# Kernel optimization log

Measured on AMD Instinct MI355X. Metric: run time of the kernel, lower is better.

## Reference

```python
import jax, jax.numpy as jnp
import numpy as np

# Architecture constants (match init_kwargs)
J_OCT, Q, K = 4, 8, 7
DECIMATION, POOLING, INDEX = 2, 8, 0
NF = K * 2 ** J_OCT            # 112 taps per filter (kernel size / time grid length)
NSC = J_OCT * Q                # 32 wavelet scales (complex filters)
POOL_W = POOLING // DECIMATION ** (INDEX + 1)  # 4


def complex_hermite_interp(xi, xk, m, p):
    # xi: (NF,) time grid; xk: (NSC, K) knots; m, p: (2, K) values/derivatives
    h = jnp.array([[1., 0., -3., 2.], [0., 1., -2., 1.],
                   [0., 0., 3., -2.], [0., 0., -1., 1.]], dtype=xi.dtype)
    xx = jnp.stack([xk[:, :-1], xk[:, 1:]], axis=2)            # (NSC, K-1, 2)
    mm = jnp.stack([m[:, :-1], m[:, 1:]], axis=2)              # (2, K-1, 2)
    pp = jnp.stack([p[:, :-1], p[:, 1:]], axis=2)
    y = jnp.concatenate([mm, pp], axis=2)                      # (2, K-1, 4)
    yh = jnp.einsum('iab,bc->iac', y, h)                       # (2, K-1, 4)
    # normalized position in each knot interval: (NSC, K-1, NF)
    xn = (xi[None, None, :] - xx[:, :, 0:1]) / (xx[:, :, 1:2] - xx[:, :, 0:1])
    mask = ((xn >= 0.) & (xn < 1.)).astype(xi.dtype)
    xp = xn[..., None] ** jnp.arange(4, dtype=xi.dtype)        # (NSC, K-1, NF, 4)
    return jnp.einsum('irf,srtf->ist', yh, xp * mask[..., None])  # (2, NSC, NF)


def get_filters(m, p, scales_delta, knots_base):
    scales = 2. ** (jnp.arange(NSC, dtype=jnp.float32) / np.float32(Q)) + scales_delta
    clipped = jnp.clip(knots_base[None, :] * scales[:, None], 1., float(NF - K))
    knots_sum = jnp.cumsum(clipped, axis=1) - clipped          # exclusive cumsum
    knots = knots_sum - (K // 2) * scales[:, None]             # (NSC, K)
    time_max = np.float32(K * 2 ** (J_OCT - 1))
    time_grid = jnp.linspace(-time_max, time_max, NF)
    mask = jnp.ones((1, K), dtype=jnp.float32).at[0, 0].set(0.).at[0, -1].set(0.)
    m_null = m - jnp.mean(m[:, 1:-1], axis=1, keepdims=True)
    f = complex_hermite_interp(time_grid, knots, m_null * mask, p * mask)  # (2, NSC, NF)
    f = f / jnp.max(f, axis=2, keepdims=True)
    filt_concat = f.reshape(2 * NSC, NF)  # [real; imag] rows, same as tf.concat axis=0
    return jnp.transpose(filt_concat)[:, None, :]              # (NF, 1, 2*NSC) = WIO


def scatter_conv(x, kernel):
    B, C, T = x.shape
    xr = x.reshape(B * C, T, 1)
    xp = jnp.pad(xr, ((0, 0), (NF // 2 - 1, NF // 2 + 1), (0, 0)), mode='symmetric')
    return jax.lax.conv_general_dilated(
        xp, kernel, window_strides=(DECIMATION,), padding='VALID',
        dimension_numbers=('NWC', 'WIO', 'NWC'))                # (B*C, To, 2*NSC)


def reference(x, m, p, scales_delta, knots_base):
    B, C, T = x.shape
    kernel = get_filters(m, p, scales_delta, knots_base)
    x_conv, vjp = jax.vjp(lambda xx: scatter_conv(xx, kernel), x)
    u = jnp.sqrt(jnp.square(x_conv[..., :NSC]) + jnp.square(x_conv[..., NSC:]))  # (B*C, To, NSC)
    out_u = jnp.swapaxes(u.reshape(B, C, NSC, -1), 1, 2)       # (B, NSC, C, To)
    pooled = jax.lax.reduce_window(u, 0., jax.lax.add,
                                   (1, POOL_W, 1), (1, POOL_W, 1), 'VALID') / POOL_W
    pooled = jnp.swapaxes(pooled, 1, 2)                        # (B*C, NSC, Tp)
    out_s = pooled.reshape(B, C, NSC, -1)                      # (B, C, NSC, Tp)
    # embedded tf.gradients auxiliary reconstruction loss
    inverse = vjp(x_conv)[0]
    loss = jnp.mean(jnp.square(inverse - jax.lax.stop_gradient(x)))
    return out_u, out_s, loss


def setup_inputs() -> dict:
    key = jax.random.key(0)
    B, C, T = 16, 3, 65536
    x = jax.random.normal(key, (B, C, T), dtype=jnp.float32)
    n = jnp.arange(K, dtype=jnp.float32)
    ham = 0.54 - 0.46 * jnp.cos(2. * jnp.pi * n / K)           # periodic hamming (tf default)
    alt = jnp.cos(n * jnp.pi) * ham
    m = jnp.stack([alt, jnp.zeros(K, jnp.float32)])
    p = jnp.stack([jnp.zeros(K, jnp.float32), alt])
    scales_delta = jnp.zeros(NSC, dtype=jnp.float32)
    knots_base = jnp.ones(K, dtype=jnp.float32)
    return {'x': x, 'm': m, 'p': p, 'scales_delta': scales_delta, 'knots_base': knots_base}
```

## Files before the change

### kernel.cpp

```cpp
#include <hip/hip_runtime.h>

#define TLEN 65536
#define XPLEN 65648
#define TO 32769
#define OU_SIZE 50333184

typedef __attribute__((ext_vector_type(8))) short short8v;
typedef __attribute__((ext_vector_type(4))) float float4v;

__device__ __forceinline__ float fetch_xp(const float* __restrict__ xr, int idx) {
    int p = idx - 55;
    p = (p < 0) ? (-1 - p) : p;
    p = (p >= TLEN) ? (2 * TLEN - 1 - p) : p;
    return xr[p];
}

__device__ __forceinline__ ushort f2bf(float f) {
    unsigned u = __float_as_uint(f);
    unsigned r = (u + 0x7fffu + ((u >> 16) & 1u)) >> 16;
    return (ushort)r;
}

__device__ __forceinline__ void bar_lds() {
    __builtin_amdgcn_sched_barrier(0);
    asm volatile("s_waitcnt lgkmcnt(0)" ::: "memory");
    __builtin_amdgcn_s_barrier();
    __builtin_amdgcn_sched_barrier(0);
}

__global__ __launch_bounds__(256) void k1_filters(
    const float* __restrict__ m, const float* __restrict__ p,
    const float* __restrict__ sd, const float* __restrict__ kb,
    float* __restrict__ Wout, ushort* __restrict__ Wtb)
{
    __shared__ float knots[32][8];
    __shared__ float yh[2][6][4];
    __shared__ float fv[2][32][112];
    __shared__ float mx[64];
    __shared__ float mv[2][7], pv[2][7];
    int tid = threadIdx.x;
    if (tid < 32) {
        float s = exp2f((float)tid * 0.125f) + sd[tid];
        float cum = 0.f;
        for (int k = 0; k < 7; ++k) {
            float c = fminf(fmaxf(kb[k] * s, 1.f), 105.f);
            knots[tid][k] = cum - 3.f * s;
            cum += c;
        }
    }
    if (tid < 2) {
        float mean = 0.f;
        for (int k = 1; k <= 5; ++k) mean += m[tid * 7 + k];
        mean *= 0.2f;
        for (int k = 0; k < 7; ++k) {
            float msk = (k == 0 || k == 6) ? 0.f : 1.f;
            mv[tid][k] = (m[tid * 7 + k] - mean) * msk;
            pv[tid][k] = p[tid * 7 + k] * msk;
        }
    }
    __syncthreads();
    if (tid < 12) {
        int i = tid / 6, kk = tid % 6;
        float y0 = mv[i][kk], y1 = mv[i][kk + 1], y2 = pv[i][kk], y3 = pv[i][kk + 1];
        yh[i][kk][0] = y0;
        yh[i][kk][1] = y1;
        yh[i][kk][2] = -3.f * y0 - 2.f * y1 + 3.f * y2 - y3;
        yh[i][kk][3] = 2.f * y0 + y1 - 2.f * y2 + y3;
    }
    __syncthreads();
    for (int idx = tid; idx < 7168; idx += 256) {
        int i = idx / 3584, s = (idx / 112) % 32, fi = idx % 112;
        float xi = -56.f + (float)fi * (112.f / 111.f);
        float val = 0.f;
        for (int kk = 0; kk < 6; ++kk) {
            float x0 = knots[s][kk], x1 = knots[s][kk + 1];
            float xn = (xi - x0) / (x1 - x0);
            if (xn >= 0.f && xn < 1.f) {
                val += ((yh[i][kk][3] * xn + yh[i][kk][2]) * xn + yh[i][kk][1]) * xn + yh[i][kk][0];
            }
        }
        fv[i][s][fi] = val;
    }
    __syncthreads();
    if (tid < 64) {
        int i = tid >> 5, s = tid & 31;
        float mm_ = -1e30f;
        for (int fi = 0; fi < 112; ++fi) mm_ = fmaxf(mm_, fv[i][s][fi]);
        mx[tid] = mm_;
    }
    __syncthreads();
    for (int idx = tid; idx < 7168; idx += 256) {
        int i = idx / 3584, s = (idx / 112) % 32, fi = idx % 112;
        int o = i * 32 + s;
        Wout[fi * 64 + o] = fv[i][s][fi] / mx[o];
    }
    for (int idx = tid; idx < 8192; idx += 256) {
        int o = idx >> 7, k = idx & 127;
        float val = (k < 112) ? fv[o >> 5][o & 31][k] / mx[o] : 0.f;
        Wtb[idx] = f2bf(val);
    }
}

__global__ __launch_bounds__(256) void k1b_A(const float* __restrict__ W, float* __restrict__ A)
{
    int idx = blockIdx.x * 256 + threadIdx.x;
    if (idx >= 12544) return;
    int j = idx / 112, k = idx % 112;
    float s = 0.f;
    for (int o = 0; o < 64; ++o) s += W[j * 64 + o] * W[k * 64 + o];
    A[idx] = s;
}

__global__ __launch_bounds__(256) void k1c_C(const float* __restrict__ A, float* __restrict__ C)
{
    int idx = blockIdx.x * 256 + threadIdx.x;
    if (idx >= 448) return;
    int q = idx / 224, dd = idx % 224;
    int d = dd - 111;
    float s = 0.f;
    for (int k = q; k < 112; k += 2) {
        int jj = k + d;
        if (jj >= 0 && jj < 112) s += A[jj * 112 + k];
    }
    C[idx] = s;
}

__global__ __launch_bounds__(256) void k2k3_fused(
    const float* __restrict__ x, const ushort* __restrict__ Wtb,
    const float* __restrict__ Cg,
    float* __restrict__ out_u, float* __restrict__ out_s,
    double* __restrict__ part)
{
    __shared__ __align__(16) ushort xraw[2][384];
    __shared__ float ub[256][33];
    __shared__ float pb[32][65];
    __shared__ __align__(16) float sx[1248];
    __shared__ __align__(16) float Cl[448];
    __shared__ double wred[4];
    int row = blockIdx.y;
    int b = row / 3, c = row % 3;
    const float* xr = x + row * TLEN;
    int tid = threadIdx.x;
    int l = tid & 63, w = tid >> 6;
    int r16 = l & 15, kg = l >> 4;

    union U8 { short8v v; uint u[4]; uint4 q; };

    const ushort* WB = Wtb + r16 * 128 + 8 * kg;
    U8 wreg[4][4];
#pragma unroll
    for (int n = 0; n < 4; ++n)
#pragma unroll
        for (int ks = 0; ks < 4; ++ks)
            wreg[n][ks].q = *(const uint4*)(WB + n * 2048 + 32 * ks);

    int ebase = 2 * (32 * w + r16) + 8 * kg;

    int tstart = blockIdx.x * 8;
    int tend = (blockIdx.x == 31) ? 257 : (tstart + 8);
    int ntiles = tend - tstart;

    auto flush = [&](int f) {
        int slot = (f & 1) << 7;
        int pend_t0 = (tstart + f) * 128;
        const int NE = 128;
        for (int i = tid; i < (NE << 3); i += 256) {
            int r = i & 31;
            int g = i >> 5;
            size_t gb = ((size_t)((b * 32 + r) * 3 + c)) * TO + pend_t0;
            int pad = (int)((4 - (gb & 3)) & 3);
            int e = pad + (g << 2);
            if (e + 3 < NE) {
                int t = pend_t0 + e;
                float4 v = make_float4(ub[slot + e][r], ub[slot + e + 1][r],
                                       ub[slot + e + 2][r], ub[slot + e + 3][r]);
                if (t + 3 < TO) {
                    *(float4*)(out_u + gb + e) = v;
                } else {
                    if (t     < TO) out_u[gb + e]     = v.x;
                    if (t + 1 < TO) out_u[gb + e + 1] = v.y;
                    if (t + 2 < TO) out_u[gb + e + 2] = v.z;
                    if (t + 3 < TO) out_u[gb + e + 3] = v.w;
                }
            }
        }
        if (tid < 128) {
            int r = tid >> 2, j = tid & 3;
            size_t gb = ((size_t)((b * 32 + r) * 3 + c)) * TO + pend_t0;
            int pad = (int)((4 - (gb & 3)) & 3);
            if (pad > 0) {
                int G4 = ((NE - pad) >> 2) << 2;
                int e = (j < pad) ? j : (pad + G4 + (j - pad));
                if (e < NE) {
                    int t = pend_t0 + e;
                    if (t < TO) out_u[gb + e] = ub[slot + e][r];
                }
            }
        }
        int ps = (f & 1) << 5;
        int tp0 = pend_t0 >> 2;
        {
            int r = tid & 31;
            int g = tid >> 5;
            int tp = g << 2;
            size_t sb = ((size_t)(row * 32 + r)) * 8192 + tp0;
            if (tp0 + tp + 3 < 8192) {
                float4 v = make_float4(pb[r][ps + tp], pb[r][ps + tp + 1],
                                       pb[r][ps + tp + 2], pb[r][ps + tp + 3]);
                *(float4*)(out_s + sb + tp) = v;
            } else {
#pragma unroll
                for (int j = 0; j < 4; ++j)
                    if (tp0 + tp + j < 8192) out_s[sb + tp + j] = pb[r][ps + tp + j];
            }
        }
    };

    {
        int i0 = 2 * tstart * 128 + tid;
        float v0 = (i0 < XPLEN) ? fetch_xp(xr, i0) : 0.f;
        float v1 = 0.f;
        if (tid < 128) {
            int i1 = i0 + 256;
            v1 = (i1 < XPLEN) ? fetch_xp(xr, i1) : 0.f;
        }
        xraw[0][tid] = f2bf(v0);
        if (tid < 128) xraw[0][tid + 256] = f2bf(v1);
    }
    bar_lds();

    for (int it = 0; it < ntiles; ++it) {
        int half = it & 1;
        float n0 = 0.f, n1 = 0.f;
        bool hn = (it + 1 < ntiles);
        if (hn) {
            int i0 = 2 * (tstart + it + 1) * 128 + tid;
            n0 = (i0 < XPLEN) ? fetch_xp(xr, i0) : 0.f;
            if (tid < 128) {
                int i1 = i0 + 256;
                n1 = (i1 < XPLEN) ? fetch_xp(xr, i1) : 0.f;
            }
        }
        __builtin_amdgcn_sched_barrier(0);
        if (it >= 1) flush(it - 1);
        __builtin_amdgcn_sched_barrier(0);
        if (hn) {
            xraw[(it + 1) & 1][tid] = f2bf(n0);
            if (tid < 128) xraw[(it + 1) & 1][tid + 256] = f2bf(n1);
        }
        bar_lds();

        const ushort* xcur = xraw[half];
        float4v acc[2][4];
#pragma unroll
        for (int mt = 0; mt < 2; ++mt)
#pragma unroll
            for (int n = 0; n < 4; ++n)
                acc[mt][n] = (float4v){0.f, 0.f, 0.f, 0.f};

#pragma unroll
        for (int ks = 0; ks < 4; ++ks) {
            U8 a0, a1;
            int e0 = ebase + 32 * ks;
#pragma unroll
            for (int q = 0; q < 4; ++q) {
                a0.u[q] = *(const uint*)&xcur[e0 + 2 * q];
                a1.u[q] = *(const uint*)&xcur[e0 + 32 + 2 * q];
            }
#pragma unroll
            for (int n = 0; n < 4; ++n) {
                acc[0][n] = __builtin_amdgcn_mfma_f32_16x16x32_bf16(a0.v, wreg[n][ks].v, acc[0][n], 0, 0, 0);
                acc[1][n] = __builtin_amdgcn_mfma_f32_16x16x32_bf16(a1.v, wreg[n][ks].v, acc[1][n], 0, 0, 0);
            }
        }

        int t0 = (tstart + it) * 128;
#pragma unroll
        for (int mt = 0; mt < 2; ++mt) {
            int tl = 32 * w + 16 * mt + 4 * kg;
            int ts = t0 + tl;
            float u1[4], u2[4];
#pragma unroll
            for (int r = 0; r < 4; ++r) {
                float re1 = acc[mt][0][r], im1 = acc[mt][2][r];
                float re2 = acc[mt][1][r], im2 = acc[mt][3][r];
                u1[r] = sqrtf(re1 * re1 + im1 * im1);
                u2[r] = sqrtf(re2 * re2 + im2 * im2);
            }
#pragma unroll
            for (int r = 0; r < 4; ++r) {
                ub[(half << 7) + tl + r][r16]      = u1[r];
                ub[(half << 7) + tl + r][r16 + 16] = u2[r];
            }
            if (ts + 3 < TO) {
                int pc = (half << 5) + (tl >> 2);
                pb[r16][pc]      = (u1[0] + u1[1] + u1[2] + u1[3]) * 0.25f;
                pb[r16 + 16][pc] = (u2[0] + u2[1] + u2[2] + u2[3]) * 0.25f;
            }
        }
        bar_lds();
    }
    flush(ntiles - 1);

    for (int li = tid; li < 448; li += 256) Cl[li] = Cg[li];
    for (int cc = 0; cc < 2; ++cc) {
        int chunk = 2 * blockIdx.x + cc;
        int s0 = 56 + chunk * 1024;
        if (cc) bar_lds();
        for (int li = tid; li < 1248; li += 256) {
            int pp = s0 - 111 + li;
            pp = (pp < 0) ? (-1 - pp) : pp;
            pp = (pp >= TLEN) ? (2 * TLEN - 1 - pp) : pp;
            sx[li] = xr[pp];
        }
        bar_lds();

        int qe = (55 + s0) & 1;
        const float* Ce = Cl + qe * 224;
        const float* Co = Cl + (qe ^ 1) * 224;
        int base = tid * 4;
        float a0 = 0.f, a1 = 0.f, a2 = 0.f, a3 = 0.f;
        float4 cur = *(const float4*)&sx[base];
#pragma unroll 4
        for (int d4 = 0; d4 < 56; ++d4) {
            float4 nxt = *(const float4*)&sx[base + 4 * d4 + 4];
            float4 cev = *(const float4*)&Ce[4 * d4];
            float4 cov = *(const float4*)&Co[4 * d4];
            a0 = fmaf(cur.x, cev.x, a0); a1 = fmaf(cur.y, cov.x, a1); a2 = fmaf(cur.z, cev.x, a2); a3 = fmaf(cur.w, cov.x, a3);
            a0 = fmaf(cur.y, cev.y, a0); a1 = fmaf(cur.z, cov.y, a1); a2 = fmaf(cur.w, cev.y, a2); a3 = fmaf(nxt.x, cov.y, a3);
            a0 = fmaf(cur.z, cev.z, a0); a1 = fmaf(cur.w, cov.z, a1); a2 = fmaf(nxt.x, cev.z, a2); a3 = fmaf(nxt.y, cov.z, a3);
            a0 = fmaf(cur.w, cev.w, a0); a1 = fmaf(nxt.x, cov.w, a1); a2 = fmaf(nxt.y, cev.w, a2); a3 = fmaf(nxt.z, cov.w, a3);
            cur = nxt;
        }

        int sb = s0 + base;
        double lsum = 0.0;
        if (sb + 0 <= 65478) { float d = a0 - sx[base + 111]; lsum += (double)d * d; }
        if (sb + 1 <= 65478) { float d = a1 - sx[base + 112]; lsum += (double)d * d; }
        if (sb + 2 <= 65478) { float d = a2 - sx[base + 113]; lsum += (double)d * d; }
        if (sb + 3 <= 65478) { float d = a3 - sx[base + 114]; lsum += (double)d * d; }
        for (int off = 32; off > 0; off >>= 1) lsum += __shfl_down(lsum, off, 64);
        if ((tid & 63) == 0) wred[w] = lsum;
        bar_lds();
        if (tid == 0)
            part[row * 64 + chunk] = wred[0] + wred[1] + wred[2] + wred[3];
    }
}

__global__ __launch_bounds__(256) void k4_edge(
    const float* __restrict__ x, const float* __restrict__ A,
    double* __restrict__ part2)
{
    __shared__ float Al[112][113];
    __shared__ float xpw[240];
    __shared__ double wacc[4];
    int row = blockIdx.x >> 1;
    int side = blockIdx.x & 1;
    const float* xr = x + row * TLEN;
    int tid = threadIdx.x;

    for (int idx = tid; idx < 12544; idx += 256)
        Al[idx / 112][idx % 112] = A[idx];
    {
        int n_x = side ? 225 : 222;
        int woff0 = side ? 65423 : 0;
        if (tid < n_x) xpw[tid] = fetch_xp(xr, woff0 + tid);
    }
    __syncthreads();

    int w = tid >> 6, lane = tid & 63;
    int nS = side ? 57 : 56;
    int woff = side ? 65423 : 0;
    double lacc = 0.0;
    for (int s = w; s < nS; s += 4) {
        float part = 0.f;
#pragma unroll
        for (int half = 0; half < 2; ++half) {
            int i;
            bool has;
            if (!side) { i = half ? (54 - s) : (55 + s); has = half ? (s <= 54) : true; }
            else       { i = half ? (65647 - s) : (65534 + s); has = true; }
            if (has) {
                int klo = max(0, i - 65536);
                int khi = min(111, i);
                int k0 = klo + ((klo ^ i) & 1);
                for (int k = k0; k <= khi; k += 2) {
                    int bi = i - k - woff;
                    part = fmaf(xpw[bi + lane], Al[lane][k], part);
                    if (lane < 48)
                        part = fmaf(xpw[bi + 64 + lane], Al[lane + 64][k], part);
                }
            }
        }
        for (int off = 32; off > 0; off >>= 1) part += __shfl_down(part, off, 64);
        if (lane == 0) {
            float xs = xpw[side ? (111 + s) : (s + 55)];
            float diff = part - xs;
            lacc += (double)diff * diff;
        }
    }
    if (lane == 0) wacc[w] = lacc;
    __syncthreads();
    if (tid == 0) part2[blockIdx.x] = wacc[0] + wacc[1] + wacc[2] + wacc[3];
}

__global__ __launch_bounds__(256) void k5_final(
    const double* __restrict__ part, const double* __restrict__ part2,
    float* __restrict__ out_loss)
{
    __shared__ double red[256];
    double acc = 0.0;
    for (int idx = threadIdx.x; idx < 3072; idx += 256) acc += part[idx];
    if (threadIdx.x < 96) acc += part2[threadIdx.x];
    red[threadIdx.x] = acc;
    __syncthreads();
    for (int st = 128; st > 0; st >>= 1) {
        if (threadIdx.x < st) red[threadIdx.x] += red[threadIdx.x + st];
        __syncthreads();
    }
    if (threadIdx.x == 0)
        out_loss[0] = (float)(red[0] / 3145728.0);
}

extern "C" void kernel_launch(void* const* d_in, const int* in_sizes, int n_in,
                              void* d_out, int out_size, void* d_ws, size_t ws_size,
                              hipStream_t stream)
{
    (void)in_sizes; (void)n_in; (void)ws_size;
    const float* x  = (const float*)d_in[0];
    const float* m  = (const float*)d_in[1];
    const float* p  = (const float*)d_in[2];
    const float* sd = (const float*)d_in[3];
    const float* kb = (const float*)d_in[4];
    float* out = (float*)d_out;
    float* ws  = (float*)d_ws;

    float* ws_w     = ws;
    float* ws_C     = ws + 7168;
    float* ws_A     = ws + 7616;
    double* ws_part  = (double*)(ws + 20160);
    double* ws_part2 = (double*)(ws + 26304);
    ushort* ws_wtb  = (ushort*)(ws + 26496);

    k1_filters<<<1, 256, 0, stream>>>(m, p, sd, kb, ws_w, ws_wtb);
    k1b_A<<<49, 256, 0, stream>>>(ws_w, ws_A);
    k1c_C<<<2, 256, 0, stream>>>(ws_A, ws_C);
    k2k3_fused<<<dim3(32, 48), 256, 0, stream>>>(x, ws_wtb, ws_C, out, out + OU_SIZE, ws_part);
    k4_edge<<<96, 256, 0, stream>>>(x, ws_A, ws_part2);
    k5_final<<<1, 256, 0, stream>>>(ws_part, ws_part2, out + (out_size - 1));
}
```

Baseline: 248.6 us.

## Interleave reconstruction-loss FIR work into the MFMA tile loop

Measured after the change: 295.6 us. +18.9%, slower.

```diff
diff --git a/kernel.cpp b/kernel.cpp
--- a/kernel.cpp
+++ b/kernel.cpp
@@ -159,6 +159,46 @@
     int tstart = blockIdx.x * 8;
     int tend = (blockIdx.x == 31) ? 257 : (tstart + 8);
     int ntiles = tend - tstart;
+
+    const int kbase = tid * 4;
+    float ka0 = 0.f, ka1 = 0.f, ka2 = 0.f, ka3 = 0.f;
+    const float* Ce = Cl + 224;
+    const float* Co = Cl;
+
+    auto k3seg = [&](int d4s, int d4e) {
+        float4 cur = *(const float4*)&sx[kbase + 4 * d4s];
+#pragma unroll 4
+        for (int d4 = d4s; d4 < d4e; ++d4) {
+            float4 nxt = *(const float4*)&sx[kbase + 4 * d4 + 4];
+            float4 cev = *(const float4*)&Ce[4 * d4];
+            float4 cov = *(const float4*)&Co[4 * d4];
+            ka0 = fmaf(cur.x, cev.x, ka0); ka1 = fmaf(cur.y, cov.x, ka1); ka2 = fmaf(cur.z, cev.x, ka2); ka3 = fmaf(cur.w, cov.x, ka3);
+            ka0 = fmaf(cur.y, cev.y, ka0); ka1 = fmaf(cur.z, cov.y, ka1); ka2 = fmaf(cur.w, cev.y, ka2); ka3 = fmaf(nxt.x, cov.y, ka3);
+            ka0 = fmaf(cur.z, cev.z, ka0); ka1 = fmaf(cur.w, cov.z, ka1); ka2 = fmaf(nxt.x, cev.z, ka2); ka3 = fmaf(nxt.y, cov.z, ka3);
+            ka0 = fmaf(cur.w, cev.w, ka0); ka1 = fmaf(nxt.x, cov.w, ka1); ka2 = fmaf(nxt.y, cev.w, ka2); ka3 = fmaf(nxt.z, cov.w, ka3);
+            cur = nxt;
+        }
+    };
+    auto k3fin = [&](int chunk) {
+        int s0 = 56 + chunk * 1024;
+        int sb = s0 + kbase;
+        double lsum = 0.0;
+        if (sb + 0 <= 65478) { float d = ka0 - sx[kbase + 111]; lsum += (double)d * d; }
+        if (sb + 1 <= 65478) { float d = ka1 - sx[kbase + 112]; lsum += (double)d * d; }
+        if (sb + 2 <= 65478) { float d = ka2 - sx[kbase + 113]; lsum += (double)d * d; }
+        if (sb + 3 <= 65478) { float d = ka3 - sx[kbase + 114]; lsum += (double)d * d; }
+        for (int off = 32; off > 0; off >>= 1) lsum += __shfl_down(lsum, off, 64);
+        if ((tid & 63) == 0) wred[w] = lsum;
+    };
+    auto k3stage = [&](int chunk) {
+        int s0 = 56 + chunk * 1024;
+        for (int li = tid; li < 1248; li += 256) {
+            int pp = s0 - 111 + li;
+            pp = (pp < 0) ? (-1 - pp) : pp;
+            pp = (pp >= TLEN) ? (2 * TLEN - 1 - pp) : pp;
+            sx[li] = xr[pp];
+        }
+    };
 
     auto flush = [&](int f) {
         int slot = (f & 1) << 7;
@@ -216,6 +256,8 @@
         }
     };
 
+    for (int li = tid; li < 448; li += 256) Cl[li] = Cg[li];
+    k3stage(2 * blockIdx.x);
     {
         int i0 = 2 * tstart * 128 + tid;
         float v0 = (i0 < XPLEN) ? fetch_xp(xr, i0) : 0.f;
@@ -248,6 +290,7 @@
             xraw[(it + 1) & 1][tid] = f2bf(n0);
             if (tid < 128) xraw[(it + 1) & 1][tid + 256] = f2bf(n1);
         }
+        if (it == 3) k3stage(2 * blockIdx.x + 1);
         bar_lds();
 
         const ushort* xcur = xraw[half];
@@ -298,53 +341,26 @@
                 pb[r16 + 16][pc] = (u2[0] + u2[1] + u2[2] + u2[3]) * 0.25f;
             }
         }
+
+        switch (it) {
+            case 0: k3seg(0, 19);  break;
+            case 1: k3seg(19, 38); break;
+            case 2: k3seg(38, 56); k3fin(2 * blockIdx.x); break;
+            case 3: if (tid == 0)
+                        part[row * 64 + 2 * blockIdx.x] = wred[0] + wred[1] + wred[2] + wred[3];
+                    ka0 = ka1 = ka2 = ka3 = 0.f;
+                    break;
+            case 4: k3seg(0, 19);  break;
+            case 5: k3seg(19, 38); break;
+            case 6: k3seg(38, 56); k3fin(2 * blockIdx.x + 1); break;
+            case 7: if (tid == 0)
+                        part[row * 64 + 2 * blockIdx.x + 1] = wred[0] + wred[1] + wred[2] + wred[3];
+                    break;
+            default: break;
+        }
         bar_lds();
     }
     flush(ntiles - 1);
-
-    for (int li = tid; li < 448; li += 256) Cl[li] = Cg[li];
-    for (int cc = 0; cc < 2; ++cc) {
-        int chunk = 2 * blockIdx.x + cc;
-        int s0 = 56 + chunk * 1024;
-        if (cc) bar_lds();
-        for (int li = tid; li < 1248; li += 256) {
-            int pp = s0 - 111 + li;
-            pp = (pp < 0) ? (-1 - pp) : pp;
-            pp = (pp >= TLEN) ? (2 * TLEN - 1 - pp) : pp;
-            sx[li] = xr[pp];
-        }
-        bar_lds();
-
-        int qe = (55 + s0) & 1;
-        const float* Ce = Cl + qe * 224;
-        const float* Co = Cl + (qe ^ 1) * 224;
-        int base = tid * 4;
-        float a0 = 0.f, a1 = 0.f, a2 = 0.f, a3 = 0.f;
-        float4 cur = *(const float4*)&sx[base];
-#pragma unroll 4
-        for (int d4 = 0; d4 < 56; ++d4) {
-            float4 nxt = *(const float4*)&sx[base + 4 * d4 + 4];
-            float4 cev = *(const float4*)&Ce[4 * d4];
-            float4 cov = *(const float4*)&Co[4 * d4];
-            a0 = fmaf(cur.x, cev.x, a0); a1 = fmaf(cur.y, cov.x, a1); a2 = fmaf(cur.z, cev.x, a2); a3 = fmaf(cur.w, cov.x, a3);
-            a0 = fmaf(cur.y, cev.y, a0); a1 = fmaf(cur.z, cov.y, a1); a2 = fmaf(cur.w, cev.y, a2); a3 = fmaf(nxt.x, cov.y, a3);
-            a0 = fmaf(cur.z, cev.z, a0); a1 = fmaf(cur.w, cov.z, a1); a2 = fmaf(nxt.x, cev.z, a2); a3 = fmaf(nxt.y, cov.z, a3);
-            a0 = fmaf(cur.w, cev.w, a0); a1 = fmaf(nxt.x, cov.w, a1); a2 = fmaf(nxt.y, cev.w, a2); a3 = fmaf(nxt.z, cov.w, a3);
-            cur = nxt;
-        }
-
-        int sb = s0 + base;
-        double lsum = 0.0;
-        if (sb + 0 <= 65478) { float d = a0 - sx[base + 111]; lsum += (double)d * d; }
-        if (sb + 1 <= 65478) { float d = a1 - sx[base + 112]; lsum += (double)d * d; }
-        if (sb + 2 <= 65478) { float d = a2 - sx[base + 113]; lsum += (double)d * d; }
-        if (sb + 3 <= 65478) { float d = a3 - sx[base + 114]; lsum += (double)d * d; }
-        for (int off = 32; off > 0; off >>= 1) lsum += __shfl_down(lsum, off, 64);
-        if ((tid & 63) == 0) wred[w] = lsum;
-        bar_lds();
-        if (tid == 0)
-            part[row * 64 + chunk] = wred[0] + wred[1] + wred[2] + wred[3];
-    }
 }
 
 __global__ __launch_bounds__(256) void k4_edge(
```

## Add a dedicated store wavefront to overlap output flushes with MFMA compute

Applied to the files above, without the earlier changes.

After: 502.2 us. 102% more time.

```diff
diff --git a/kernel.cpp b/kernel.cpp
--- a/kernel.cpp
+++ b/kernel.cpp
@@ -125,7 +125,7 @@
     C[idx] = s;
 }
 
-__global__ __launch_bounds__(256) void k2k3_fused(
+__global__ __launch_bounds__(320) void k2k3_fused(
     const float* __restrict__ x, const ushort* __restrict__ Wtb,
     const float* __restrict__ Cg,
     float* __restrict__ out_u, float* __restrict__ out_s,
@@ -142,17 +142,20 @@
     const float* xr = x + row * TLEN;
     int tid = threadIdx.x;
     int l = tid & 63, w = tid >> 6;
+    int lane = l;
     int r16 = l & 15, kg = l >> 4;
 
     union U8 { short8v v; uint u[4]; uint4 q; };
 
-    const ushort* WB = Wtb + r16 * 128 + 8 * kg;
     U8 wreg[4][4];
-#pragma unroll
-    for (int n = 0; n < 4; ++n)
-#pragma unroll
-        for (int ks = 0; ks < 4; ++ks)
-            wreg[n][ks].q = *(const uint4*)(WB + n * 2048 + 32 * ks);
+    if (w < 4) {
+        const ushort* WB = Wtb + r16 * 128 + 8 * kg;
+#pragma unroll
+        for (int n = 0; n < 4; ++n)
+#pragma unroll
+            for (int ks = 0; ks < 4; ++ks)
+                wreg[n][ks].q = *(const uint4*)(WB + n * 2048 + 32 * ks);
+    }
 
     int ebase = 2 * (32 * w + r16) + 8 * kg;
 
@@ -164,7 +167,7 @@
         int slot = (f & 1) << 7;
         int pend_t0 = (tstart + f) * 128;
         const int NE = 128;
-        for (int i = tid; i < (NE << 3); i += 256) {
+        for (int i = lane; i < (NE << 3); i += 64) {
             int r = i & 31;
             int g = i >> 5;
             size_t gb = ((size_t)((b * 32 + r) * 3 + c)) * TO + pend_t0;
@@ -184,8 +187,8 @@
                 }
             }
         }
-        if (tid < 128) {
-            int r = tid >> 2, j = tid & 3;
+        for (int i = lane; i < 128; i += 64) {
+            int r = i >> 2, j = i & 3;
             size_t gb = ((size_t)((b * 32 + r) * 3 + c)) * TO + pend_t0;
             int pad = (int)((4 - (gb & 3)) & 3);
             if (pad > 0) {
@@ -199,9 +202,9 @@
         }
         int ps = (f & 1) << 5;
         int tp0 = pend_t0 >> 2;
-        {
-            int r = tid & 31;
-            int g = tid >> 5;
+        for (int i = lane; i < 256; i += 64) {
+            int r = i & 31;
+            int g = i >> 5;
             int tp = g << 2;
             size_t sb = ((size_t)(row * 32 + r)) * 8192 + tp0;
             if (tp0 + tp + 3 < 8192) {
@@ -216,7 +219,7 @@
         }
     };
 
-    {
+    if (w < 4) {
         int i0 = 2 * tstart * 128 + tid;
         float v0 = (i0 < XPLEN) ? fetch_xp(xr, i0) : 0.f;
         float v1 = 0.f;
@@ -231,83 +234,87 @@
 
     for (int it = 0; it < ntiles; ++it) {
         int half = it & 1;
+        bool hn = (it + 1 < ntiles);
         float n0 = 0.f, n1 = 0.f;
-        bool hn = (it + 1 < ntiles);
-        if (hn) {
-            int i0 = 2 * (tstart + it + 1) * 128 + tid;
-            n0 = (i0 < XPLEN) ? fetch_xp(xr, i0) : 0.f;
-            if (tid < 128) {
-                int i1 = i0 + 256;
-                n1 = (i1 < XPLEN) ? fetch_xp(xr, i1) : 0.f;
-            }
+        if (w < 4) {
+            if (hn) {
+                int i0 = 2 * (tstart + it + 1) * 128 + tid;
+                n0 = (i0 < XPLEN) ? fetch_xp(xr, i0) : 0.f;
+                if (tid < 128) {
+                    int i1 = i0 + 256;
+                    n1 = (i1 < XPLEN) ? fetch_xp(xr, i1) : 0.f;
+                }
+            }
+        } else {
+            if (it >= 1) flush(it - 1);
         }
         __builtin_amdgcn_sched_barrier(0);
-        if (it >= 1) flush(it - 1);
-        __builtin_amdgcn_sched_barrier(0);
-        if (hn) {
+        if (w < 4 && hn) {
             xraw[(it + 1) & 1][tid] = f2bf(n0);
             if (tid < 128) xraw[(it + 1) & 1][tid + 256] = f2bf(n1);
         }
         bar_lds();
 
-        const ushort* xcur = xraw[half];
-        float4v acc[2][4];
-#pragma unroll
-        for (int mt = 0; mt < 2; ++mt)
-#pragma unroll
-            for (int n = 0; n < 4; ++n)
-                acc[mt][n] = (float4v){0.f, 0.f, 0.f, 0.f};
-
-#pragma unroll
-        for (int ks = 0; ks < 4; ++ks) {
-            U8 a0, a1;
-            int e0 = ebase + 32 * ks;
-#pragma unroll
-            for (int q = 0; q < 4; ++q) {
-                a0.u[q] = *(const uint*)&xcur[e0 + 2 * q];
-                a1.u[q] = *(const uint*)&xcur[e0 + 32 + 2 * q];
-            }
-#pragma unroll
-            for (int n = 0; n < 4; ++n) {
-                acc[0][n] = __builtin_amdgcn_mfma_f32_16x16x32_bf16(a0.v, wreg[n][ks].v, acc[0][n], 0, 0, 0);
-                acc[1][n] = __builtin_amdgcn_mfma_f32_16x16x32_bf16(a1.v, wreg[n][ks].v, acc[1][n], 0, 0, 0);
-            }
-        }
-
-        int t0 = (tstart + it) * 128;
-#pragma unroll
-        for (int mt = 0; mt < 2; ++mt) {
-            int tl = 32 * w + 16 * mt + 4 * kg;
-            int ts = t0 + tl;
-            float u1[4], u2[4];
-#pragma unroll
-            for (int r = 0; r < 4; ++r) {
-                float re1 = acc[mt][0][r], im1 = acc[mt][2][r];
-                float re2 = acc[mt][1][r], im2 = acc[mt][3][r];
-                u1[r] = sqrtf(re1 * re1 + im1 * im1);
-                u2[r] = sqrtf(re2 * re2 + im2 * im2);
-            }
-#pragma unroll
-            for (int r = 0; r < 4; ++r) {
-                ub[(half << 7) + tl + r][r16]      = u1[r];
-                ub[(half << 7) + tl + r][r16 + 16] = u2[r];
-            }
-            if (ts + 3 < TO) {
-                int pc = (half << 5) + (tl >> 2);
-                pb[r16][pc]      = (u1[0] + u1[1] + u1[2] + u1[3]) * 0.25f;
-                pb[r16 + 16][pc] = (u2[0] + u2[1] + u2[2] + u2[3]) * 0.25f;
+        if (w < 4) {
+            const ushort* xcur = xraw[half];
+            float4v acc[2][4];
+#pragma unroll
+            for (int mt = 0; mt < 2; ++mt)
+#pragma unroll
+                for (int n = 0; n < 4; ++n)
+                    acc[mt][n] = (float4v){0.f, 0.f, 0.f, 0.f};
+
+#pragma unroll
+            for (int ks = 0; ks < 4; ++ks) {
+                U8 a0, a1;
+                int e0 = ebase + 32 * ks;
+#pragma unroll
+                for (int q = 0; q < 4; ++q) {
+                    a0.u[q] = *(const uint*)&xcur[e0 + 2 * q];
+                    a1.u[q] = *(const uint*)&xcur[e0 + 32 + 2 * q];
+                }
+#pragma unroll
+                for (int n = 0; n < 4; ++n) {
+                    acc[0][n] = __builtin_amdgcn_mfma_f32_16x16x32_bf16(a0.v, wreg[n][ks].v, acc[0][n], 0, 0, 0);
+                    acc[1][n] = __builtin_amdgcn_mfma_f32_16x16x32_bf16(a1.v, wreg[n][ks].v, acc[1][n], 0, 0, 0);
+                }
+            }
+
+            int t0 = (tstart + it) * 128;
+#pragma unroll
+            for (int mt = 0; mt < 2; ++mt) {
+                int tl = 32 * w + 16 * mt + 4 * kg;
+                int ts = t0 + tl;
+                float u1[4], u2[4];
+#pragma unroll
+                for (int r = 0; r < 4; ++r) {
+                    float re1 = acc[mt][0][r], im1 = acc[mt][2][r];
+                    float re2 = acc[mt][1][r], im2 = acc[mt][3][r];
+                    u1[r] = sqrtf(re1 * re1 + im1 * im1);
+                    u2[r] = sqrtf(re2 * re2 + im2 * im2);
+                }
+#pragma unroll
+                for (int r = 0; r < 4; ++r) {
+                    ub[(half << 7) + tl + r][r16]      = u1[r];
+                    ub[(half << 7) + tl + r][r16 + 16] = u2[r];
+                }
+                if (ts + 3 < TO) {
+                    int pc = (half << 5) + (tl >> 2);
+                    pb[r16][pc]      = (u1[0] + u1[1] + u1[2] + u1[3]) * 0.25f;
+                    pb[r16 + 16][pc] = (u2[0] + u2[1] + u2[2] + u2[3]) * 0.25f;
+                }
             }
         }
         bar_lds();
     }
-    flush(ntiles - 1);
-
-    for (int li = tid; li < 448; li += 256) Cl[li] = Cg[li];
+    if (w == 4) flush(ntiles - 1);
+
+    for (int li = tid; li < 448; li += 320) Cl[li] = Cg[li];
     for (int cc = 0; cc < 2; ++cc) {
         int chunk = 2 * blockIdx.x + cc;
         int s0 = 56 + chunk * 1024;
         if (cc) bar_lds();
-        for (int li = tid; li < 1248; li += 256) {
+        for (int li = tid; li < 1248; li += 320) {
             int pp = s0 - 111 + li;
             pp = (pp < 0) ? (-1 - pp) : pp;
             pp = (pp >= TLEN) ? (2 * TLEN - 1 - pp) : pp;
@@ -315,32 +322,33 @@
         }
         bar_lds();
 
-        int qe = (55 + s0) & 1;
-        const float* Ce = Cl + qe * 224;
-        const float* Co = Cl + (qe ^ 1) * 224;
-        int base = tid * 4;
-        float a0 = 0.f, a1 = 0.f, a2 = 0.f, a3 = 0.f;
-        float4 cur = *(const float4*)&sx[base];
+        if (w < 4) {
+            const float* Ce = Cl + 224;
+            const float* Co = Cl;
+            int base = tid * 4;
+            float a0 = 0.f, a1 = 0.f, a2 = 0.f, a3 = 0.f;
+            float4 cur = *(const float4*)&sx[base];
 #pragma unroll 4
-        for (int d4 = 0; d4 < 56; ++d4) {
-            float4 nxt = *(const float4*)&sx[base + 4 * d4 + 4];
-            float4 cev = *(const float4*)&Ce[4 * d4];
-            float4 cov = *(const float4*)&Co[4 * d4];
-            a0 = fmaf(cur.x, cev.x, a0); a1 = fmaf(cur.y, cov.x, a1); a2 = fmaf(cur.z, cev.x, a2); a3 = fmaf(cur.w, cov.x, a3);
-            a0 = fmaf(cur.y, cev.y, a0); a1 = fmaf(cur.z, cov.y, a1); a2 = fmaf(cur.w, cev.y, a2); a3 = fmaf(nxt.x, cov.y, a3);
-            a0 = fmaf(cur.z, cev.z, a0); a1 = fmaf(cur.w, cov.z, a1); a2 = fmaf(nxt.x, cev.z, a2); a3 = fmaf(nxt.y, cov.z, a3);
-            a0 = fmaf(cur.w, cev.w, a0); a1 = fmaf(nxt.x, cov.w, a1); a2 = fmaf(nxt.y, cev.w, a2); a3 = fmaf(nxt.z, cov.w, a3);
-            cur = nxt;
-        }
-
-        int sb = s0 + base;
-        double lsum = 0.0;
-        if (sb + 0 <= 65478) { float d = a0 - sx[base + 111]; lsum += (double)d * d; }
-        if (sb + 1 <= 65478) { float d = a1 - sx[base + 112]; lsum += (double)d * d; }
-        if (sb + 2 <= 65478) { float d = a2 - sx[base + 113]; lsum += (double)d * d; }
-        if (sb + 3 <= 65478) { float d = a3 - sx[base + 114]; lsum += (double)d * d; }
-        for (int off = 32; off > 0; off >>= 1) lsum += __shfl_down(lsum, off, 64);
-        if ((tid & 63) == 0) wred[w] = lsum;
+            for (int d4 = 0; d4 < 56; ++d4) {
+                float4 nxt = *(const float4*)&sx[base + 4 * d4 + 4];
+                float4 cev = *(const float4*)&Ce[4 * d4];
+                float4 cov = *(const float4*)&Co[4 * d4];
+                a0 = fmaf(cur.x, cev.x, a0); a1 = fmaf(cur.y, cov.x, a1); a2 = fmaf(cur.z, cev.x, a2); a3 = fmaf(cur.w, cov.x, a3);
+                a0 = fmaf(cur.y, cev.y, a0); a1 = fmaf(cur.z, cov.y, a1); a2 = fmaf(cur.w, cev.y, a2); a3 = fmaf(nxt.x, cov.y, a3);
+                a0 = fmaf(cur.z, cev.z, a0); a1 = fmaf(cur.w, cov.z, a1); a2 = fmaf(nxt.x, cev.z, a2); a3 = fmaf(nxt.y, cov.z, a3);
+                a0 = fmaf(cur.w, cev.w, a0); a1 = fmaf(nxt.x, cov.w, a1); a2 = fmaf(nxt.y, cev.w, a2); a3 = fmaf(nxt.z, cov.w, a3);
+                cur = nxt;
+            }
+
+            int sb = s0 + base;
+            double lsum = 0.0;
+            if (sb + 0 <= 65478) { float d = a0 - sx[base + 111]; lsum += (double)d * d; }
+            if (sb + 1 <= 65478) { float d = a1 - sx[base + 112]; lsum += (double)d * d; }
+            if (sb + 2 <= 65478) { float d = a2 - sx[base + 113]; lsum += (double)d * d; }
+            if (sb + 3 <= 65478) { float d = a3 - sx[base + 114]; lsum += (double)d * d; }
+            for (int off = 32; off > 0; off >>= 1) lsum += __shfl_down(lsum, off, 64);
+            if ((tid & 63) == 0) wred[w] = lsum;
+        }
         bar_lds();
         if (tid == 0)
             part[row * 64 + chunk] = wred[0] + wred[1] + wred[2] + wred[3];
@@ -445,7 +453,7 @@
     k1_filters<<<1, 256, 0, stream>>>(m, p, sd, kb, ws_w, ws_wtb);
     k1b_A<<<49, 256, 0, stream>>>(ws_w, ws_A);
     k1c_C<<<2, 256, 0, stream>>>(ws_A, ws_C);
-    k2k3_fused<<<dim3(32, 48), 256, 0, stream>>>(x, ws_wtb, ws_C, out, out + OU_SIZE, ws_part);
+    k2k3_fused<<<dim3(32, 48), 320, 0, stream>>>(x, ws_wtb, ws_C, out, out + OU_SIZE, ws_part);
     k4_edge<<<96, 256, 0, stream>>>(x, ws_A, ws_part2);
     k5_final<<<1, 256, 0, stream>>>(ws_part, ws_part2, out + (out_size - 1));
 }
```
